# Optimization experiments

Hardware: AMD Instinct MI355X
Metric: run time of the kernel (lower is better)

## Reference

```python
import jax, jax.numpy as jnp
import numpy as np

B, N, D = 2, 2048, 1024
H = 16
HD = D // H  # head_dim = 64
EPS = 1e-5


def _layernorm(x, gamma, beta):
    mu = jnp.mean(x, axis=-1, keepdims=True)
    var = jnp.var(x, axis=-1, keepdims=True)
    return (x - mu) * jax.lax.rsqrt(var + EPS) * gamma + beta


def setup_inputs() -> dict:
    key = jax.random.key(0)
    ks = jax.random.split(key, 13)
    s = 1.0 / np.sqrt(D)
    return {
        "query": jax.random.normal(ks[0], (B, N, D), dtype=jnp.float32),
        "Wq": jax.random.uniform(ks[1], (D, D), jnp.float32, -s, s),
        "bq": jax.random.uniform(ks[2], (D,), jnp.float32, -s, s),
        "Wk": jax.random.uniform(ks[3], (D, D), jnp.float32, -s, s),
        "bk": jax.random.uniform(ks[4], (D,), jnp.float32, -s, s),
        "Wv": jax.random.uniform(ks[5], (D, D), jnp.float32, -s, s),
        "bv": jax.random.uniform(ks[6], (D,), jnp.float32, -s, s),
        "Wp": jax.random.uniform(ks[7], (D, D), jnp.float32, -s, s),
        "bp": jax.random.uniform(ks[8], (D,), jnp.float32, -s, s),
        "q_gamma": jnp.ones((HD,), jnp.float32),
        "q_beta": jnp.zeros((HD,), jnp.float32),
        "k_gamma": jnp.ones((HD,), jnp.float32),
        "k_beta": jnp.zeros((HD,), jnp.float32),
    }


def reference(query, Wq, bq, Wk, bk, Wv, bv, Wp, bp, q_gamma, q_beta, k_gamma, k_beta):
    # Linear projections (torch Linear: x @ W.T + b)
    def split_heads(x):  # [B,N,D] -> [B,H,N,HD]
        return x.reshape(B, N, H, HD).transpose(0, 2, 1, 3)

    Q = split_heads(query @ Wq.T + bq)
    K = split_heads(query @ Wk.T + bk)
    V = split_heads(query @ Wv.T + bv)

    # per-head QK LayerNorm
    Q = _layernorm(Q, q_gamma, q_beta)
    K = _layernorm(K, k_gamma, k_beta)

    scale = 1.0 / np.sqrt(HD)
    attn = jax.nn.softmax(jnp.einsum('bhqd,bhkd->bhqk', Q, K) * scale, axis=-1)
    # dropout_prob = 0.0 -> identity
    out = jnp.einsum('bhqk,bhkd->bqhd', attn, V).reshape(B, N, D)
    return out @ Wp.T + bp
```

## Files before the change

### kernel.cpp

```cpp
#include <hip/hip_runtime.h>
#include <math.h>

#define Bb 2
#define Nn 2048
#define Dd 1024
#define Hh 16
#define HD 64

typedef __attribute__((ext_vector_type(8))) short short8;
typedef __attribute__((ext_vector_type(4))) short short4v;
typedef __attribute__((ext_vector_type(4))) float floatx4;

__device__ __forceinline__ short f2bf(float x) {
    unsigned u = __float_as_uint(x);
    u += 0x7fffu + ((u >> 16) & 1u);
    return (short)(u >> 16);
}

#if defined(__has_builtin)
#  if __has_builtin(__builtin_amdgcn_mfma_f32_16x16x16bf16_1k)
#    define MFMA16(a, b, c) __builtin_amdgcn_mfma_f32_16x16x16bf16_1k(a, b, c, 0, 0, 0)
#  endif
#endif
#ifndef MFMA16
static __device__ __forceinline__ floatx4 mfma16_asm(short4v a, short4v b, floatx4 c) {
    asm volatile("v_mfma_f32_16x16x16_bf16 %0, %1, %2, %0" : "+v"(c) : "v"(a), "v"(b));
    return c;
}
#  define MFMA16(a, b, c) mfma16_asm(a, b, c)
#endif

__device__ __forceinline__ float fexp2(float x) {
#if defined(__has_builtin)
#  if __has_builtin(__builtin_amdgcn_exp2f)
    return __builtin_amdgcn_exp2f(x);
#  else
    return exp2f(x);
#  endif
#else
    return exp2f(x);
#endif
}

__device__ __forceinline__ void gload16(const void* g, void* l) {
    __builtin_amdgcn_global_load_lds(
        (const __attribute__((address_space(1))) unsigned int*)g,
        (__attribute__((address_space(3))) unsigned int*)l,
        16, 0, 0);
}

#define QSCALE 0.18033688011112042f

__global__ __launch_bounds__(256) void cast_all(
    const float* __restrict__ x,
    const float* __restrict__ Wq, const float* __restrict__ Wk,
    const float* __restrict__ Wv, const float* __restrict__ Wp,
    short* __restrict__ xh, short* __restrict__ Wqh, short* __restrict__ Wkh,
    short* __restrict__ Wvh, short* __restrict__ Wph)
{
    const float* src; short* dst; int n4;
    switch (blockIdx.y) {
        case 0:  src = x;  dst = xh;  n4 = (Bb * Nn * Dd) / 4; break;
        case 1:  src = Wq; dst = Wqh; n4 = (Dd * Dd) / 4; break;
        case 2:  src = Wk; dst = Wkh; n4 = (Dd * Dd) / 4; break;
        case 3:  src = Wv; dst = Wvh; n4 = (Dd * Dd) / 4; break;
        default: src = Wp; dst = Wph; n4 = (Dd * Dd) / 4; break;
    }
    const int i = blockIdx.x * 256 + threadIdx.x;
    if (i >= n4) return;
    float4 v = ((const float4*)src)[i];
    short4v o;
    o.x = f2bf(v.x); o.y = f2bf(v.y); o.z = f2bf(v.z); o.w = f2bf(v.w);
    ((short4v*)dst)[i] = o;
}

__global__ __launch_bounds__(256) void qkv_ln_gemm(
    const short* __restrict__ xh,
    const short* __restrict__ Wqh, const short* __restrict__ Wkh,
    const short* __restrict__ Wvh,
    const float* __restrict__ bq, const float* __restrict__ bk,
    const float* __restrict__ bv,
    const float* __restrict__ qg, const float* __restrict__ qb,
    const float* __restrict__ kg, const float* __restrict__ kb,
    short* __restrict__ Qh, short* __restrict__ Kh, short* __restrict__ Vt)
{
    const int z = blockIdx.z;
    const short* A; const short* W;
    int rowBase, colBase, Nc;
    if (z < 2) { A = xh;  W = z ? Wkh : Wqh;
                 rowBase = blockIdx.x * 128; colBase = blockIdx.y * 128; Nc = Dd; }
    else       { A = Wvh; W = xh;
                 rowBase = blockIdx.y * 128; colBase = blockIdx.x * 128; Nc = Bb * Nn; }

    __shared__ __align__(16) short As[128 * 32];
    __shared__ __align__(16) short Ws[128 * 32];

    const int t    = threadIdx.x;
    const int w    = t >> 6;
    const int lane = t & 63;
    const int quad = lane >> 4;
    const int l15  = lane & 15;
    const int wy   = w >> 1;
    const int wx   = w & 1;

    const int r0 = t >> 2;
    const int kg4 = (t & 3) * 8;
    const short* aP = A + (size_t)(rowBase + r0) * Dd + kg4;
    const short* wP = W + (size_t)(colBase + r0) * Dd + kg4;
    const size_t rowskip = (size_t)64 * Dd;

    floatx4 acc[4][4];
    #pragma unroll
    for (int mi = 0; mi < 4; ++mi)
        #pragma unroll
        for (int ni = 0; ni < 4; ++ni)
            acc[mi][ni] = (floatx4){0.f, 0.f, 0.f, 0.f};

    for (int k0 = 0; k0 < Dd; k0 += 32) {
        gload16(aP,           &As[t * 8]);
        gload16(aP + rowskip, &As[(t + 256) * 8]);
        gload16(wP,           &Ws[t * 8]);
        gload16(wP + rowskip, &Ws[(t + 256) * 8]);
        aP += 32; wP += 32;
        __syncthreads();

        short8 af[4], bfr[4];
        #pragma unroll
        for (int i = 0; i < 4; ++i) {
            af[i]  = *(const short8*)&As[(wy * 64 + i * 16 + l15) * 32 + quad * 8];
            bfr[i] = *(const short8*)&Ws[(wx * 64 + i * 16 + l15) * 32 + quad * 8];
        }
        #pragma unroll
        for (int mi = 0; mi < 4; ++mi)
            #pragma unroll
            for (int ni = 0; ni < 4; ++ni)
                acc[mi][ni] = __builtin_amdgcn_mfma_f32_16x16x32_bf16(
                    af[mi], bfr[ni], acc[mi][ni], 0, 0, 0);
        __syncthreads();
    }

    if (z == 2) {
        #pragma unroll
        for (int mi = 0; mi < 4; ++mi) {
            #pragma unroll
            for (int r = 0; r < 4; ++r) {
                const size_t row = rowBase + wy * 64 + mi * 16 + quad * 4 + r;
                const float brv = bv[row];
                #pragma unroll
                for (int ni = 0; ni < 4; ++ni) {
                    const int col = colBase + wx * 64 + ni * 16 + l15;
                    Vt[row * (size_t)Nc + col] = f2bf(acc[mi][ni][r] + brv);
                }
            }
        }
    } else {
        const float* bias = z ? bk : bq;
        const float* gam  = z ? kg : qg;
        const float* bet  = z ? kb : qb;
        const float oscale = z ? 1.0f : QSCALE;
        short* out = z ? Kh : Qh;
        float bcol[4], g4[4], be4[4];
        #pragma unroll
        for (int ni = 0; ni < 4; ++ni) {
            const int ch = ni * 16 + l15;
            bcol[ni] = bias[colBase + wx * 64 + ch];
            g4[ni]   = gam[ch];
            be4[ni]  = bet[ch];
        }
        #pragma unroll
        for (int mi = 0; mi < 4; ++mi) {
            #pragma unroll
            for (int r = 0; r < 4; ++r) {
                const size_t row = rowBase + wy * 64 + mi * 16 + quad * 4 + r;
                float v[4], s = 0.f, s2 = 0.f;
                #pragma unroll
                for (int ni = 0; ni < 4; ++ni) {
                    v[ni] = acc[mi][ni][r] + bcol[ni];
                    s += v[ni]; s2 += v[ni] * v[ni];
                }
                #pragma unroll
                for (int d = 1; d < 16; d <<= 1) {
                    s  += __shfl_xor(s,  d, 16);
                    s2 += __shfl_xor(s2, d, 16);
                }
                const float mean = s * (1.0f / 64.0f);
                const float var  = s2 * (1.0f / 64.0f) - mean * mean;
                const float rr   = rsqrtf(var + 1e-5f);
                #pragma unroll
                for (int ni = 0; ni < 4; ++ni) {
                    const int col = colBase + wx * 64 + ni * 16 + l15;
                    out[row * (size_t)Dd + col] =
                        f2bf(((v[ni] - mean) * rr * g4[ni] + be4[ni]) * oscale);
                }
            }
        }
    }
}

__global__ __launch_bounds__(256) void gemm_mfma(
    const short* __restrict__ A, const short* __restrict__ W,
    const float* __restrict__ bias, float* __restrict__ Cf,
    int M, int K, int Nc)
{
    __shared__ __align__(16) short As[128 * 32];
    __shared__ __align__(16) short Ws[128 * 32];

    const int t    = threadIdx.x;
    const int w    = t >> 6;
    const int lane = t & 63;
    const int quad = lane >> 4;
    const int l15  = lane & 15;
    const int wy   = w >> 1;
    const int wx   = w & 1;
    const int rowBase = blockIdx.y * 128;
    const int colBase = blockIdx.x * 128;

    const int r0 = t >> 2;
    const int kg4 = (t & 3) * 8;
    const short* aP = A + (size_t)(rowBase + r0) * K + kg4;
    const short* wP = W + (size_t)(colBase + r0) * K + kg4;
    const size_t rowskip = (size_t)64 * K;

    floatx4 acc[4][4];
    #pragma unroll
    for (int mi = 0; mi < 4; ++mi)
        #pragma unroll
        for (int ni = 0; ni < 4; ++ni)
            acc[mi][ni] = (floatx4){0.f, 0.f, 0.f, 0.f};

    for (int k0 = 0; k0 < K; k0 += 32) {
        gload16(aP,           &As[t * 8]);
        gload16(aP + rowskip, &As[(t + 256) * 8]);
        gload16(wP,           &Ws[t * 8]);
        gload16(wP + rowskip, &Ws[(t + 256) * 8]);
        aP += 32; wP += 32;
        __syncthreads();

        short8 af[4], bfr[4];
        #pragma unroll
        for (int i = 0; i < 4; ++i) {
            af[i]  = *(const short8*)&As[(wy * 64 + i * 16 + l15) * 32 + quad * 8];
            bfr[i] = *(const short8*)&Ws[(wx * 64 + i * 16 + l15) * 32 + quad * 8];
        }
        #pragma unroll
        for (int mi = 0; mi < 4; ++mi)
            #pragma unroll
            for (int ni = 0; ni < 4; ++ni)
                acc[mi][ni] = __builtin_amdgcn_mfma_f32_16x16x32_bf16(
                    af[mi], bfr[ni], acc[mi][ni], 0, 0, 0);
        __syncthreads();
    }

    #pragma unroll
    for (int mi = 0; mi < 4; ++mi) {
        #pragma unroll
        for (int r = 0; r < 4; ++r) {
            const size_t row = rowBase + wy * 64 + mi * 16 + quad * 4 + r;
            #pragma unroll
            for (int ni = 0; ni < 4; ++ni) {
                const int col = colBase + wx * 64 + ni * 16 + l15;
                Cf[row * Nc + col] = acc[mi][ni][r] + bias[col];
            }
        }
    }
}

__global__ __launch_bounds__(512, 4) void flash_mfma(
    const short* __restrict__ Qh, const short* __restrict__ Kh,
    const short* __restrict__ Vt, short* __restrict__ ctx)
{
    const int qt = blockIdx.x;
    const int h  = blockIdx.y;
    const int b  = blockIdx.z;

    const int t    = threadIdx.x;
    const int w    = t >> 6;
    const int lane = t & 63;
    const int quad = lane >> 4;
    const int l15  = lane & 15;

    __shared__ __align__(16) short Ksh[64][72];
    __shared__ __align__(16) short Vsh[64][76];

    const size_t bhead = (size_t)b * Nn * Dd + (size_t)h * HD;

    short8 qf[2];
    {
        const short* qp = Qh + bhead
            + (size_t)(qt * 128 + w * 16 + l15) * Dd + quad * 8;
        qf[0] = *(const short8*)qp;
        qf[1] = *(const short8*)(qp + 32);
    }

    floatx4 accO[4], accL;
    #pragma unroll
    for (int n = 0; n < 4; ++n) accO[n] = (floatx4){0.f, 0.f, 0.f, 0.f};
    accL = (floatx4){0.f, 0.f, 0.f, 0.f};
    short4v ones;
    ones[0] = ones[1] = ones[2] = ones[3] = (short)0x3F80;

    const int s3  = t >> 3;
    const int c3  = ((t & 7) + (s3 & 7)) & 7;
    const int skg = c3 * 8;
    const short* kP = Kh + bhead + (size_t)s3 * Dd + skg;
    const short* vP = Vt + (size_t)(h * 64 + s3) * (Bb * Nn) + (size_t)b * Nn + skg;

    short8 kr = *(const short8*)kP;
    short8 vr = *(const short8*)vP;

    for (int k0 = 0; k0 < Nn; k0 += 64) {
        *(short8*)&Ksh[s3][skg] = kr;
        {
            union { short8 v8; short4v v4[2]; } vv; vv.v8 = vr;
            *(short4v*)&Vsh[s3][skg]     = vv.v4[0];
            *(short4v*)&Vsh[s3][skg + 4] = vv.v4[1];
        }
        __syncthreads();

        kP += 64 * Dd; vP += 64;
        kr = *(const short8*)kP;
        vr = *(const short8*)vP;

        floatx4 accS[4];
        __builtin_amdgcn_s_setprio(1);
        #pragma unroll
        for (int n = 0; n < 4; ++n) {
            short8 kf0 = *(const short8*)&Ksh[n * 16 + l15][quad * 8];
            short8 kf1 = *(const short8*)&Ksh[n * 16 + l15][32 + quad * 8];
            floatx4 zz = (floatx4){0.f, 0.f, 0.f, 0.f};
            zz = __builtin_amdgcn_mfma_f32_16x16x32_bf16(kf0, qf[0], zz, 0, 0, 0);
            zz = __builtin_amdgcn_mfma_f32_16x16x32_bf16(kf1, qf[1], zz, 0, 0, 0);
            accS[n] = zz;
        }
        __builtin_amdgcn_s_setprio(0);

        short4v pfrag[4];
        #pragma unroll
        for (int n = 0; n < 4; ++n) {
            const unsigned u0 = __float_as_uint(fexp2(accS[n][0]));
            const unsigned u1 = __float_as_uint(fexp2(accS[n][1]));
            const unsigned u2 = __float_as_uint(fexp2(accS[n][2]));
            const unsigned u3 = __float_as_uint(fexp2(accS[n][3]));
            union { uint2 u; short4v s; } pk;
            pk.u.x = __builtin_amdgcn_perm(u1, u0, 0x07060302u);
            pk.u.y = __builtin_amdgcn_perm(u3, u2, 0x07060302u);
            pfrag[n] = pk.s;
            accL = MFMA16(pk.s, ones, accL);
        }

        __builtin_amdgcn_s_setprio(1);
        #pragma unroll
        for (int n = 0; n < 4; ++n) {
            #pragma unroll
            for (int c = 0; c < 4; ++c) {
                const short4v vb =
                    *(const short4v*)&Vsh[c * 16 + l15][n * 16 + quad * 4];
                accO[c] = MFMA16(pfrag[n], vb, accO[c]);
            }
        }
        __builtin_amdgcn_s_setprio(0);
        __syncthreads();
    }

    #pragma unroll
    for (int r = 0; r < 4; ++r) {
        const float lr = 1.0f / accL[r];
        short* dst = ctx + (size_t)((b * Nn) + qt * 128 + w * 16
                                    + quad * 4 + r) * Dd + h * HD + l15;
        #pragma unroll
        for (int n = 0; n < 4; ++n) dst[n * 16] = f2bf(accO[n][r] * lr);
    }
}

extern "C" void kernel_launch(void* const* d_in, const int* in_sizes, int n_in,
                              void* d_out, int out_size, void* d_ws, size_t ws_size,
                              hipStream_t stream) {
    const float* x   = (const float*)d_in[0];
    const float* Wq  = (const float*)d_in[1];
    const float* bq  = (const float*)d_in[2];
    const float* Wk  = (const float*)d_in[3];
    const float* bk  = (const float*)d_in[4];
    const float* Wv  = (const float*)d_in[5];
    const float* bv  = (const float*)d_in[6];
    const float* Wp  = (const float*)d_in[7];
    const float* bp  = (const float*)d_in[8];
    const float* qg  = (const float*)d_in[9];
    const float* qb  = (const float*)d_in[10];
    const float* kg  = (const float*)d_in[11];
    const float* kb  = (const float*)d_in[12];
    float* out = (float*)d_out;

    const size_t S = (size_t)Bb * Nn * Dd;
    short* wsb = (short*)d_ws;
    short* xh   = wsb;
    short* Vt   = wsb + S;
    short* Kh   = wsb + 2 * S;
    short* Qh   = wsb + 3 * S;
    short* ctxh = wsb + 4 * S;
    short* Wqh  = wsb + 5 * S;
    short* Wkh  = Wqh + Dd * Dd;
    short* Wvh  = Wkh + Dd * Dd;
    short* Wph  = Wvh + Dd * Dd;

    const int M = Bb * Nn;

    cast_all<<<dim3(4096, 5), 256, 0, stream>>>(x, Wq, Wk, Wv, Wp,
                                                xh, Wqh, Wkh, Wvh, Wph);

    qkv_ln_gemm<<<dim3(M / 128, Dd / 128, 3), 256, 0, stream>>>(
        xh, Wqh, Wkh, Wvh, bq, bk, bv, qg, qb, kg, kb, Qh, Kh, Vt);

    flash_mfma<<<dim3(Nn / 128, Hh, Bb), 512, 0, stream>>>(Qh, Kh, Vt, ctxh);

    gemm_mfma<<<dim3(Dd / 128, M / 128, 1), 256, 0, stream>>>(
        ctxh, Wph, bp, out, M, Dd, Dd);
}
```

Baseline: 222.0 us.

## Double KV tile per flash iteration and narrow output-projection GEMM tiles

The flash attention kernel now stages 128 keys/values per iteration instead of 64. This halves the number of barriers and loop trips, and it fuses the exp/pack step into the per-16-key MFMA loop instead of running it as separate passes. The output projection GEMM switches to 128x64 tiles, doubling the block count (256 to 512) to fill more CUs. The cost is more LDS in flash, more register pressure from double prefetch, and lower arithmetic intensity per GEMM block.

```diff
diff --git a/kernel.cpp b/kernel.cpp
--- a/kernel.cpp
+++ b/kernel.cpp
@@ -6,6 +6,7 @@
 #define Dd 1024
 #define Hh 16
 #define HD 64
+#define KVB 128
 
 typedef __attribute__((ext_vector_type(8))) short short8;
 typedef __attribute__((ext_vector_type(4))) short short4v;
@@ -203,7 +204,7 @@
     int M, int K, int Nc)
 {
     __shared__ __align__(16) short As[128 * 32];
-    __shared__ __align__(16) short Ws[128 * 32];
+    __shared__ __align__(16) short Ws[64 * 32];
 
     const int t    = threadIdx.x;
     const int w    = t >> 6;
@@ -213,7 +214,7 @@
     const int wy   = w >> 1;
     const int wx   = w & 1;
     const int rowBase = blockIdx.y * 128;
-    const int colBase = blockIdx.x * 128;
+    const int colBase = blockIdx.x * 64;
 
     const int r0 = t >> 2;
     const int kg4 = (t & 3) * 8;
@@ -221,31 +222,31 @@
     const short* wP = W + (size_t)(colBase + r0) * K + kg4;
     const size_t rowskip = (size_t)64 * K;
 
-    floatx4 acc[4][4];
+    floatx4 acc[4][2];
     #pragma unroll
     for (int mi = 0; mi < 4; ++mi)
         #pragma unroll
-        for (int ni = 0; ni < 4; ++ni)
+        for (int ni = 0; ni < 2; ++ni)
             acc[mi][ni] = (floatx4){0.f, 0.f, 0.f, 0.f};
 
     for (int k0 = 0; k0 < K; k0 += 32) {
         gload16(aP,           &As[t * 8]);
         gload16(aP + rowskip, &As[(t + 256) * 8]);
         gload16(wP,           &Ws[t * 8]);
-        gload16(wP + rowskip, &Ws[(t + 256) * 8]);
         aP += 32; wP += 32;
         __syncthreads();
 
-        short8 af[4], bfr[4];
-        #pragma unroll
-        for (int i = 0; i < 4; ++i) {
+        short8 af[4], bfr[2];
+        #pragma unroll
+        for (int i = 0; i < 4; ++i)
             af[i]  = *(const short8*)&As[(wy * 64 + i * 16 + l15) * 32 + quad * 8];
-            bfr[i] = *(const short8*)&Ws[(wx * 64 + i * 16 + l15) * 32 + quad * 8];
-        }
+        #pragma unroll
+        for (int i = 0; i < 2; ++i)
+            bfr[i] = *(const short8*)&Ws[(wx * 32 + i * 16 + l15) * 32 + quad * 8];
         #pragma unroll
         for (int mi = 0; mi < 4; ++mi)
             #pragma unroll
-            for (int ni = 0; ni < 4; ++ni)
+            for (int ni = 0; ni < 2; ++ni)
                 acc[mi][ni] = __builtin_amdgcn_mfma_f32_16x16x32_bf16(
                     af[mi], bfr[ni], acc[mi][ni], 0, 0, 0);
         __syncthreads();
@@ -257,8 +258,8 @@
         for (int r = 0; r < 4; ++r) {
             const size_t row = rowBase + wy * 64 + mi * 16 + quad * 4 + r;
             #pragma unroll
-            for (int ni = 0; ni < 4; ++ni) {
-                const int col = colBase + wx * 64 + ni * 16 + l15;
+            for (int ni = 0; ni < 2; ++ni) {
+                const int col = colBase + wx * 32 + ni * 16 + l15;
                 Cf[row * Nc + col] = acc[mi][ni][r] + bias[col];
             }
         }
@@ -279,8 +280,8 @@
     const int quad = lane >> 4;
     const int l15  = lane & 15;
 
-    __shared__ __align__(16) short Ksh[64][72];
-    __shared__ __align__(16) short Vsh[64][76];
+    __shared__ __align__(16) short Ksh[KVB][72];
+    __shared__ __align__(16) short Vsh[64][140];
 
     const size_t bhead = (size_t)b * Nn * Dd + (size_t)h * HD;
 
@@ -303,59 +304,55 @@
     const int c3  = ((t & 7) + (s3 & 7)) & 7;
     const int skg = c3 * 8;
     const short* kP = Kh + bhead + (size_t)s3 * Dd + skg;
-    const short* vP = Vt + (size_t)(h * 64 + s3) * (Bb * Nn) + (size_t)b * Nn + skg;
-
-    short8 kr = *(const short8*)kP;
-    short8 vr = *(const short8*)vP;
-
-    for (int k0 = 0; k0 < Nn; k0 += 64) {
-        *(short8*)&Ksh[s3][skg] = kr;
+    const short* vP = Vt + (size_t)(h * 64 + s3) * (size_t)(Bb * Nn) + (size_t)b * Nn + skg;
+
+    short8 kr0 = *(const short8*)kP;
+    short8 kr1 = *(const short8*)(kP + (size_t)64 * Dd);
+    short8 vr0 = *(const short8*)vP;
+    short8 vr1 = *(const short8*)(vP + 64);
+
+    for (int k0 = 0; k0 < Nn; k0 += KVB) {
+        *(short8*)&Ksh[s3][skg]      = kr0;
+        *(short8*)&Ksh[s3 + 64][skg] = kr1;
         {
-            union { short8 v8; short4v v4[2]; } vv; vv.v8 = vr;
-            *(short4v*)&Vsh[s3][skg]     = vv.v4[0];
-            *(short4v*)&Vsh[s3][skg + 4] = vv.v4[1];
-        }
-        __syncthreads();
-
-        kP += 64 * Dd; vP += 64;
-        kr = *(const short8*)kP;
-        vr = *(const short8*)vP;
-
-        floatx4 accS[4];
+            union { short8 v8; short4v v4[2]; } a0, a1;
+            a0.v8 = vr0; a1.v8 = vr1;
+            *(short4v*)&Vsh[s3][skg]      = a0.v4[0];
+            *(short4v*)&Vsh[s3][skg + 4]  = a0.v4[1];
+            *(short4v*)&Vsh[s3][skg + 64] = a1.v4[0];
+            *(short4v*)&Vsh[s3][skg + 68] = a1.v4[1];
+        }
+        __syncthreads();
+
+        kP += (size_t)KVB * Dd; vP += KVB;
+        kr0 = *(const short8*)kP;
+        kr1 = *(const short8*)(kP + (size_t)64 * Dd);
+        vr0 = *(const short8*)vP;
+        vr1 = *(const short8*)(vP + 64);
+
         __builtin_amdgcn_s_setprio(1);
         #pragma unroll
-        for (int n = 0; n < 4; ++n) {
+        for (int n = 0; n < KVB / 16; ++n) {
             short8 kf0 = *(const short8*)&Ksh[n * 16 + l15][quad * 8];
             short8 kf1 = *(const short8*)&Ksh[n * 16 + l15][32 + quad * 8];
             floatx4 zz = (floatx4){0.f, 0.f, 0.f, 0.f};
             zz = __builtin_amdgcn_mfma_f32_16x16x32_bf16(kf0, qf[0], zz, 0, 0, 0);
             zz = __builtin_amdgcn_mfma_f32_16x16x32_bf16(kf1, qf[1], zz, 0, 0, 0);
-            accS[n] = zz;
-        }
-        __builtin_amdgcn_s_setprio(0);
-
-        short4v pfrag[4];
-        #pragma unroll
-        for (int n = 0; n < 4; ++n) {
-            const unsigned u0 = __float_as_uint(fexp2(accS[n][0]));
-            const unsigned u1 = __float_as_uint(fexp2(accS[n][1]));
-            const unsigned u2 = __float_as_uint(fexp2(accS[n][2]));
-            const unsigned u3 = __float_as_uint(fexp2(accS[n][3]));
+
+            const unsigned u0 = __float_as_uint(fexp2(zz[0]));
+            const unsigned u1 = __float_as_uint(fexp2(zz[1]));
+            const unsigned u2 = __float_as_uint(fexp2(zz[2]));
+            const unsigned u3 = __float_as_uint(fexp2(zz[3]));
             union { uint2 u; short4v s; } pk;
             pk.u.x = __builtin_amdgcn_perm(u1, u0, 0x07060302u);
             pk.u.y = __builtin_amdgcn_perm(u3, u2, 0x07060302u);
-            pfrag[n] = pk.s;
             accL = MFMA16(pk.s, ones, accL);
-        }
-
-        __builtin_amdgcn_s_setprio(1);
-        #pragma unroll
-        for (int n = 0; n < 4; ++n) {
+
             #pragma unroll
             for (int c = 0; c < 4; ++c) {
                 const short4v vb =
                     *(const short4v*)&Vsh[c * 16 + l15][n * 16 + quad * 4];
-                accO[c] = MFMA16(pfrag[n], vb, accO[c]);
+                accO[c] = MFMA16(pk.s, vb, accO[c]);
             }
         }
         __builtin_amdgcn_s_setprio(0);
@@ -412,6 +409,6 @@
 
     flash_mfma<<<dim3(Nn / 128, Hh, Bb), 512, 0, stream>>>(Qh, Kh, Vt, ctxh);
 
-    gemm_mfma<<<dim3(Dd / 128, M / 128, 1), 256, 0, stream>>>(
+    gemm_mfma<<<dim3(Dd / 64, M / 128, 1), 256, 0, stream>>>(
         ctxh, Wph, bp, out, M, Dd, Dd);
 }
```

After: 218.6 us. No clear change (-1.6%).
